# Optimization experiments

Measured on AMD Instinct MI355X. Metric: run time of the kernel, lower is better.

The kernel has to match this reference:

```python
import jax, jax.numpy as jnp
import numpy as np

DIM = 2048
SEQ = 8192
NUM_HEADS = 16
PROJ_DIM = DIM // 4  # proj_ratio = 4.0
EPS = 1e-5


def setup_inputs() -> dict:
    key = jax.random.key(0)
    ks = jax.random.split(key, 8)
    s = 0.02  # param init scale
    return {
        "x": jax.random.normal(ks[0], (SEQ, DIM), jnp.float32),
        "q": jax.random.normal(ks[1], (1, DIM), jnp.float32),
        "W_kv": jax.random.normal(ks[2], (2 * DIM, DIM), jnp.float32) * s,
        "b_kv": jax.random.normal(ks[3], (2 * DIM,), jnp.float32) * s,
        "W_p1": jax.random.normal(ks[4], (PROJ_DIM, DIM), jnp.float32) * s,
        "b_p1": jax.random.normal(ks[5], (PROJ_DIM,), jnp.float32) * s,
        "W_p2": jax.random.normal(ks[6], (DIM, PROJ_DIM), jnp.float32) * s,
        "b_p2": jax.random.normal(ks[7], (DIM,), jnp.float32) * s,
        "ln_w": jnp.ones((PROJ_DIM,), jnp.float32),
        "ln_b": jnp.zeros((PROJ_DIM,), jnp.float32),
    }


def reference(x, q, W_kv, b_kv, W_p1, b_p1, W_p2, b_p2, ln_w, ln_b):
    seq, dim = x.shape
    h = NUM_HEADS
    d = dim // h

    # kv projection: [s, 2*dim]; split '(n h d)' with n leading -> k = first dim cols
    kv = x @ W_kv.T + b_kv
    k = kv[:, :dim].reshape(seq, h, d).transpose(1, 0, 2)   # [h, s, d]
    v = kv[:, dim:].reshape(seq, h, d).transpose(1, 0, 2)   # [h, s, d]
    qh = q.reshape(h, 1, d)                                  # '1 (h d) -> h 1 d'

    # single-query attention (qk_norm=False -> Identity norms)
    attn = jnp.einsum('hqd,hkd->hqk', qh, k) / jnp.sqrt(jnp.asarray(d, x.dtype))
    attn = jax.nn.softmax(attn, axis=-1)                     # [h, 1, s]
    x1 = jnp.einsum('hqk,hkd->hqd', attn, v)                 # [h, 1, d]
    x1 = x1.transpose(1, 0, 2).reshape(1, dim)               # 'h s d -> s (h d)'

    # proj MLP: proj1 -> LayerNorm -> relu -> proj2
    h1 = x1 @ W_p1.T + b_p1                                  # [1, proj_dim]
    mu = jnp.mean(h1, axis=-1, keepdims=True)
    var = jnp.mean(jnp.square(h1 - mu), axis=-1, keepdims=True)
    h1 = (h1 - mu) / jnp.sqrt(var + EPS) * ln_w + ln_b
    x1 = jax.nn.relu(h1) @ W_p2.T + b_p2                     # [1, dim]

    # residual broadcast: [s, dim] + [1, dim]
    return x + x1
```

## Files before the change

### kernel.cpp

```cpp
#include <hip/hip_runtime.h>
#include <math.h>

#define SEQ   8192
#define DIM   2048
#define NH    16
#define DH    128
#define PD    512

static constexpr float LN_EPS = 1e-5f;
static constexpr float SCALE  = 0.08838834764831845f;

typedef __bf16 bf16x8 __attribute__((ext_vector_type(8)));
typedef float  f32x4  __attribute__((ext_vector_type(4)));

static constexpr size_t OFF_QB   = 0;
static constexpr size_t OFF_SMP  = 16;
static constexpr size_t OFF_QWB  = 528;
static constexpr size_t OFF_PCTX = 16912;
static constexpr size_t OFF_CTX  = OFF_PCTX + 8388608;
static constexpr size_t OFF_X1   = OFF_CTX + 32768;
static constexpr size_t OFF_H1R  = OFF_X1 + 2048;
static constexpr size_t OFF_X1F  = OFF_H1R + 512;

__device__ __forceinline__ void gload_lds16(const float* g, float* l) {
    __builtin_amdgcn_global_load_lds(
        (const __attribute__((address_space(1))) uint32_t*)g,
        (__attribute__((address_space(3))) uint32_t*)l,
        16, 0, 0);
}

__global__ __launch_bounds__(256) void k_prep(const float* __restrict__ q,
                                              const float* __restrict__ Wkv,
                                              const float* __restrict__ bkv,
                                              __bf16* __restrict__ qWb,
                                              float* __restrict__ qb,
                                              float* __restrict__ smp) {
    int t = threadIdx.x;
    int h = blockIdx.x >> 4, jc = blockIdx.x & 15;
    int col = t & 127, kh = t >> 7;
    int j = jc * 128 + col;
    const float* w  = Wkv + (size_t)(h * DH + kh * 64) * DIM + j;
    const float* qh = q + h * DH + kh * 64;
    float acc = 0.f;
#pragma unroll 16
    for (int d = 0; d < 64; ++d)
        acc += qh[d] * __builtin_nontemporal_load(w + (size_t)d * DIM);
    __shared__ float part[128];
    if (kh) part[col] = acc;
    __syncthreads();
    if (!kh) qWb[h * DIM + j] = (__bf16)(acc + part[col]);
    if (jc == 0 && t < 64) {
        float p = q[h*DH + t] * bkv[h*DH + t] + q[h*DH + 64 + t] * bkv[h*DH + 64 + t];
        for (int off = 32; off; off >>= 1) p += __shfl_down(p, off);
        if (t == 0) qb[h] = p;
    }
    if (blockIdx.x == 0) { smp[t] = 0.f; smp[t + 256] = 0.f; }
}

#define ROWF 2052
__global__ __launch_bounds__(512) void k_fctx(const float* __restrict__ x,
                                              const __bf16* __restrict__ qWb,
                                              const float* __restrict__ qb,
                                              float* __restrict__ pctx,
                                              float* __restrict__ smp) {
    const int b = blockIdx.x, t = threadIdx.x;
    const int w8 = t >> 6, lane = t & 63;
    const int s0 = b * 32;
    const int r = lane & 15, quad = lane >> 4;

    __shared__ float ldsx[16 * ROWF];
    __shared__ float dpart[8][64][4];
    __shared__ float att[16][NH];
    __shared__ float hsum[NH];
    if (t < NH) hsum[t] = 0.f;

    const int kbase = w8 * 256;
    const int j0 = t * 4;
    f32x4 acc4[NH];
#pragma unroll
    for (int h = 0; h < NH; ++h) acc4[h] = (f32x4){0.f, 0.f, 0.f, 0.f};

    for (int h2 = 0; h2 < 2; ++h2) {
        if (h2) __syncthreads();
        {
            const float* gsrc = x + (size_t)(s0 + h2 * 16) * DIM + kbase + lane * 4;
            float*       ldst = ldsx + kbase + lane * 4;
#pragma unroll
            for (int i = 0; i < 16; ++i)
                gload_lds16(gsrc + (size_t)i * DIM, ldst + i * ROWF);
        }
        asm volatile("s_waitcnt vmcnt(0)" ::: "memory");
        __syncthreads();

        {
            const __bf16* brow = qWb + r * DIM + kbase + quad * 8;
            const float*  lrow = ldsx + r * ROWF + kbase + quad * 8;
            f32x4 acc = {0.f, 0.f, 0.f, 0.f};
#pragma unroll
            for (int i = 0; i < 8; ++i) {
                f32x4 xa = *(const f32x4*)(lrow + i * 32);
                f32x4 xb = *(const f32x4*)(lrow + i * 32 + 4);
                bf16x8 af;
                af[0] = (__bf16)xa[0]; af[1] = (__bf16)xa[1];
                af[2] = (__bf16)xa[2]; af[3] = (__bf16)xa[3];
                af[4] = (__bf16)xb[0]; af[5] = (__bf16)xb[1];
                af[6] = (__bf16)xb[2]; af[7] = (__bf16)xb[3];
                bf16x8 bv = *(const bf16x8*)(brow + i * 32);
                acc = __builtin_amdgcn_mfma_f32_16x16x32_bf16(af, bv, acc, 0, 0, 0);
            }
            *(f32x4*)&dpart[w8][lane][0] = acc;
        }
        __syncthreads();

        if (t < 256) {
            const int h = t & 15, sl = t >> 4;
            const int quad2 = sl >> 2, reg2 = sl & 3;
            const int lane2 = quad2 * 16 + h;
            float v = 0.f;
#pragma unroll
            for (int kk = 0; kk < 8; ++kk) v += dpart[kk][lane2][reg2];
            float e = __expf((v + qb[h]) * SCALE);
            att[sl][h] = e;
            atomicAdd(&hsum[h], e);
        }
        __syncthreads();

#pragma unroll 4
        for (int rr = 0; rr < 16; ++rr) {
            f32x4 xv = *(const f32x4*)(ldsx + rr * ROWF + j0);
            const f32x4* ar = (const f32x4*)att[rr];
            f32x4 a0 = ar[0], a1 = ar[1], a2 = ar[2], a3 = ar[3];
            float aa[16];
            *(f32x4*)&aa[0] = a0; *(f32x4*)&aa[4]  = a1;
            *(f32x4*)&aa[8] = a2; *(f32x4*)&aa[12] = a3;
#pragma unroll
            for (int h = 0; h < NH; ++h) acc4[h] += xv * aa[h];
        }
    }

    if (t < NH) atomicAdd(&smp[t * 32 + (b & 31)], hsum[t]);
#pragma unroll
    for (int h = 0; h < NH; ++h)
        __builtin_nontemporal_store(acc4[h],
            (f32x4*)&pctx[((size_t)(b * NH + h)) * DIM + j0]);
}
#undef ROWF

__global__ __launch_bounds__(256) void k_ctxred(const float* __restrict__ pctx,
                                                const float* __restrict__ smp,
                                                float* __restrict__ ctx) {
    const int b = blockIdx.x, t = threadIdx.x;
    const int h = b >> 5;
    const int col = t & 63, ch = t >> 6;
    __shared__ float sInv;
    __shared__ float psum[4][64];
    const size_t idx = (size_t)b * 64 + col;
    const int c0 = ch * 64;
    float s = 0.f;
#pragma unroll 16
    for (int c = 0; c < 64; ++c)
        s += __builtin_nontemporal_load(&pctx[(size_t)(c0 + c) * (NH * DIM) + idx]);
    psum[ch][col] = s;
    if (t < 32) {
        float v = smp[h * 32 + t];
        for (int off = 16; off; off >>= 1) v += __shfl_xor(v, off);
        if (t == 0) sInv = 1.0f / v;
    }
    __syncthreads();
    if (ch == 0)
        ctx[idx] = (psum[0][col] + psum[1][col] + psum[2][col] + psum[3][col]) * sInv;
}

__global__ __launch_bounds__(256) void k_x1(const float* __restrict__ Wkv,
                                            const float* __restrict__ bkv,
                                            const float* __restrict__ ctx,
                                            float* __restrict__ x1) {
    int row = blockIdx.x * 4 + (threadIdx.x >> 6);
    int lane = threadIdx.x & 63;
    const float* w = Wkv + (size_t)(DIM + row) * DIM;
    const float* c = ctx + (row >> 7) * DIM;
    float acc = 0.f;
#pragma unroll
    for (int k = 0; k < 8; ++k) {
        int j = k * 256 + lane * 4;
        f32x4 wv = __builtin_nontemporal_load((const f32x4*)&w[j]);
        f32x4 cv = *(const f32x4*)&c[j];
        acc += wv[0]*cv[0] + wv[1]*cv[1] + wv[2]*cv[2] + wv[3]*cv[3];
    }
    for (int off = 32; off; off >>= 1) acc += __shfl_xor(acc, off);
    if (lane == 0) x1[row] = acc + bkv[DIM + row];
}

__global__ __launch_bounds__(256) void k_h1(const float* __restrict__ Wp1,
                                            const float* __restrict__ bp1,
                                            const float* __restrict__ x1,
                                            float* __restrict__ h1raw) {
    int row = blockIdx.x * 4 + (threadIdx.x >> 6);
    int lane = threadIdx.x & 63;
    const float* w = Wp1 + (size_t)row * DIM;
    float acc = 0.f;
#pragma unroll
    for (int k = 0; k < 8; ++k) {
        int j = k * 256 + lane * 4;
        f32x4 wv = __builtin_nontemporal_load((const f32x4*)&w[j]);
        f32x4 cv = *(const f32x4*)&x1[j];
        acc += wv[0]*cv[0] + wv[1]*cv[1] + wv[2]*cv[2] + wv[3]*cv[3];
    }
    for (int off = 32; off; off >>= 1) acc += __shfl_xor(acc, off);
    if (lane == 0) h1raw[row] = acc + bp1[row];
}

__global__ __launch_bounds__(256) void k_x1f(const float* __restrict__ Wp2,
                                             const float* __restrict__ bp2,
                                             const float* __restrict__ h1raw,
                                             const float* __restrict__ lnw,
                                             const float* __restrict__ lnb,
                                             float* __restrict__ x1f) {
    int row = blockIdx.x * 4 + (threadIdx.x >> 6);
    int lane = threadIdx.x & 63;
    int j = lane * 8;
    float4 va = *(const float4*)&h1raw[j];
    float4 vb = *(const float4*)&h1raw[j + 4];
    float s = va.x + va.y + va.z + va.w + vb.x + vb.y + vb.z + vb.w;
    for (int off = 32; off; off >>= 1) s += __shfl_xor(s, off);
    float mu = s * (1.0f / PD);
    float dx[8];
    dx[0]=va.x-mu; dx[1]=va.y-mu; dx[2]=va.z-mu; dx[3]=va.w-mu;
    dx[4]=vb.x-mu; dx[5]=vb.y-mu; dx[6]=vb.z-mu; dx[7]=vb.w-mu;
    float s2 = 0.f;
#pragma unroll
    for (int i = 0; i < 8; ++i) s2 += dx[i] * dx[i];
    for (int off = 32; off; off >>= 1) s2 += __shfl_xor(s2, off);
    float rstd = rsqrtf(s2 * (1.0f / PD) + LN_EPS);
    float4 lw0 = *(const float4*)&lnw[j], lw1 = *(const float4*)&lnw[j + 4];
    float4 lb0 = *(const float4*)&lnb[j], lb1 = *(const float4*)&lnb[j + 4];
    float hln[8];
    hln[0]=fmaxf(dx[0]*rstd*lw0.x+lb0.x,0.f); hln[1]=fmaxf(dx[1]*rstd*lw0.y+lb0.y,0.f);
    hln[2]=fmaxf(dx[2]*rstd*lw0.z+lb0.z,0.f); hln[3]=fmaxf(dx[3]*rstd*lw0.w+lb0.w,0.f);
    hln[4]=fmaxf(dx[4]*rstd*lw1.x+lb1.x,0.f); hln[5]=fmaxf(dx[5]*rstd*lw1.y+lb1.y,0.f);
    hln[6]=fmaxf(dx[6]*rstd*lw1.z+lb1.z,0.f); hln[7]=fmaxf(dx[7]*rstd*lw1.w+lb1.w,0.f);
    const float* w = Wp2 + (size_t)row * PD + j;
    f32x4 w0 = __builtin_nontemporal_load((const f32x4*)w);
    f32x4 w1 = __builtin_nontemporal_load((const f32x4*)(w + 4));
    float acc = w0[0]*hln[0] + w0[1]*hln[1] + w0[2]*hln[2] + w0[3]*hln[3]
              + w1[0]*hln[4] + w1[1]*hln[5] + w1[2]*hln[6] + w1[3]*hln[7];
    for (int off = 32; off; off >>= 1) acc += __shfl_xor(acc, off);
    if (lane == 0) x1f[row] = acc + bp2[row];
}

__global__ __launch_bounds__(256) void k_out(const float* __restrict__ x,
                                             const float* __restrict__ x1f,
                                             float* __restrict__ out) {
    size_t i = (size_t)blockIdx.x * 512 + threadIdx.x;
    f32x4 xv = ((const f32x4*)x)[i];
    f32x4 a  = ((const f32x4*)x1f)[(int)(i & 511)];
    __builtin_nontemporal_store(xv + a, (f32x4*)out + i);
    size_t i2 = i + 256;
    f32x4 xv2 = ((const f32x4*)x)[i2];
    f32x4 a2  = ((const f32x4*)x1f)[(int)(i2 & 511)];
    __builtin_nontemporal_store(xv2 + a2, (f32x4*)out + i2);
}

extern "C" void kernel_launch(void* const* d_in, const int* in_sizes, int n_in,
                              void* d_out, int out_size, void* d_ws, size_t ws_size,
                              hipStream_t stream) {
    const float* x    = (const float*)d_in[0];
    const float* q    = (const float*)d_in[1];
    const float* Wkv  = (const float*)d_in[2];
    const float* bkv  = (const float*)d_in[3];
    const float* Wp1  = (const float*)d_in[4];
    const float* bp1  = (const float*)d_in[5];
    const float* Wp2  = (const float*)d_in[6];
    const float* bp2  = (const float*)d_in[7];
    const float* lnw  = (const float*)d_in[8];
    const float* lnb  = (const float*)d_in[9];
    float* out = (float*)d_out;
    float* ws  = (float*)d_ws;

    float*  qb    = ws + OFF_QB;
    float*  smp   = ws + OFF_SMP;
    __bf16* qWb   = (__bf16*)(ws + OFF_QWB);
    float*  pctx  = ws + OFF_PCTX;
    float*  ctx   = ws + OFF_CTX;
    float*  x1    = ws + OFF_X1;
    float*  h1raw = ws + OFF_H1R;
    float*  x1f   = ws + OFF_X1F;

    k_prep  <<<256, 256, 0, stream>>>(q, Wkv, bkv, qWb, qb, smp);
    k_fctx  <<<256, 512, 0, stream>>>(x, qWb, qb, pctx, smp);
    k_ctxred<<<512, 256, 0, stream>>>(pctx, smp, ctx);
    k_x1    <<<512, 256, 0, stream>>>(Wkv, bkv, ctx, x1);
    k_h1    <<<128, 256, 0, stream>>>(Wp1, bp1, x1, h1raw);
    k_x1f   <<<512, 256, 0, stream>>>(Wp2, bp2, h1raw, lnw, lnb, x1f);
    k_out   <<<8192, 256, 0, stream>>>(x, x1f, out);
}
```

Before: 206.7 us.

## Double-buffer x tiles in LDS and hoist qW operands into registers

The fused context kernel now splits each 32-row block into four 8-row stages and keeps two LDS buffers. While one stage is consumed by the MFMA score computation and the weighted accumulation, the next stage is fetched with async global-to-LDS loads, so memory latency overlaps with compute instead of stalling on a full wait each half. The bf16 qW operand is loaded once into registers rather than re-read each pass. The MFMA now carries duplicated rows, so half its work is wasted. Barriers per block and register pressure also go up.

Measured after the change: 204.1 us. Within noise of the previous version (-1.3%).

```diff
diff --git a/kernel.cpp b/kernel.cpp
--- a/kernel.cpp
+++ b/kernel.cpp
@@ -28,6 +28,11 @@
         (__attribute__((address_space(3))) uint32_t*)l,
         16, 0, 0);
 }
+
+#define LBAR() do {                                        \
+    asm volatile("s_waitcnt lgkmcnt(0)" ::: "memory");     \
+    __builtin_amdgcn_s_barrier();                          \
+} while (0)
 
 __global__ __launch_bounds__(256) void k_prep(const float* __restrict__ q,
                                               const float* __restrict__ Wkv,
@@ -68,33 +73,50 @@
     const int s0 = b * 32;
     const int r = lane & 15, quad = lane >> 4;
 
-    __shared__ float ldsx[16 * ROWF];
+    __shared__ float buf[2][8 * ROWF];
     __shared__ float dpart[8][64][4];
-    __shared__ float att[16][NH];
+    __shared__ float att[8][NH];
     __shared__ float hsum[NH];
     if (t < NH) hsum[t] = 0.f;
 
     const int kbase = w8 * 256;
     const int j0 = t * 4;
+
+    bf16x8 BV[8];
+    {
+        const __bf16* brow = qWb + r * DIM + kbase + quad * 8;
+#pragma unroll
+        for (int i = 0; i < 8; ++i) BV[i] = *(const bf16x8*)(brow + i * 32);
+    }
+
     f32x4 acc4[NH];
 #pragma unroll
     for (int h = 0; h < NH; ++h) acc4[h] = (f32x4){0.f, 0.f, 0.f, 0.f};
 
-    for (int h2 = 0; h2 < 2; ++h2) {
-        if (h2) __syncthreads();
+    {
+        const float* gsrc = x + (size_t)s0 * DIM + kbase + lane * 4;
+        float*       ldst = &buf[0][0] + kbase + lane * 4;
+#pragma unroll
+        for (int i = 0; i < 8; ++i)
+            gload_lds16(gsrc + (size_t)i * DIM, ldst + i * ROWF);
+    }
+
+#pragma unroll
+    for (int s = 0; s < 4; ++s) {
+        float* cbuf = &buf[s & 1][0];
+        if (s < 3) {
+            const float* gsrc = x + (size_t)(s0 + (s + 1) * 8) * DIM + kbase + lane * 4;
+            float*       ldst = &buf[(s + 1) & 1][0] + kbase + lane * 4;
+#pragma unroll
+            for (int i = 0; i < 8; ++i)
+                gload_lds16(gsrc + (size_t)i * DIM, ldst + i * ROWF);
+            asm volatile("s_waitcnt vmcnt(8)" ::: "memory");
+        } else {
+            asm volatile("s_waitcnt vmcnt(0)" ::: "memory");
+        }
+
         {
-            const float* gsrc = x + (size_t)(s0 + h2 * 16) * DIM + kbase + lane * 4;
-            float*       ldst = ldsx + kbase + lane * 4;
-#pragma unroll
-            for (int i = 0; i < 16; ++i)
-                gload_lds16(gsrc + (size_t)i * DIM, ldst + i * ROWF);
-        }
-        asm volatile("s_waitcnt vmcnt(0)" ::: "memory");
-        __syncthreads();
-
-        {
-            const __bf16* brow = qWb + r * DIM + kbase + quad * 8;
-            const float*  lrow = ldsx + r * ROWF + kbase + quad * 8;
+            const float* lrow = cbuf + (r & 7) * ROWF + kbase + quad * 8;
             f32x4 acc = {0.f, 0.f, 0.f, 0.f};
 #pragma unroll
             for (int i = 0; i < 8; ++i) {
@@ -105,14 +127,13 @@
                 af[2] = (__bf16)xa[2]; af[3] = (__bf16)xa[3];
                 af[4] = (__bf16)xb[0]; af[5] = (__bf16)xb[1];
                 af[6] = (__bf16)xb[2]; af[7] = (__bf16)xb[3];
-                bf16x8 bv = *(const bf16x8*)(brow + i * 32);
-                acc = __builtin_amdgcn_mfma_f32_16x16x32_bf16(af, bv, acc, 0, 0, 0);
+                acc = __builtin_amdgcn_mfma_f32_16x16x32_bf16(af, BV[i], acc, 0, 0, 0);
             }
             *(f32x4*)&dpart[w8][lane][0] = acc;
         }
-        __syncthreads();
-
-        if (t < 256) {
+        LBAR();
+
+        if (t < 128) {
             const int h = t & 15, sl = t >> 4;
             const int quad2 = sl >> 2, reg2 = sl & 3;
             const int lane2 = quad2 * 16 + h;
@@ -123,11 +144,11 @@
             att[sl][h] = e;
             atomicAdd(&hsum[h], e);
         }
-        __syncthreads();
-
-#pragma unroll 4
-        for (int rr = 0; rr < 16; ++rr) {
-            f32x4 xv = *(const f32x4*)(ldsx + rr * ROWF + j0);
+        LBAR();
+
+#pragma unroll 2
+        for (int rr = 0; rr < 8; ++rr) {
+            f32x4 xv = *(const f32x4*)(cbuf + rr * ROWF + j0);
             const f32x4* ar = (const f32x4*)att[rr];
             f32x4 a0 = ar[0], a1 = ar[1], a2 = ar[2], a3 = ar[3];
             float aa[16];
@@ -136,6 +157,7 @@
 #pragma unroll
             for (int h = 0; h < NH; ++h) acc4[h] += xv * aa[h];
         }
+        LBAR();
     }
 
     if (t < NH) atomicAdd(&smp[t * 32 + (b & 31)], hsum[t]);
```
